# Kernel tuning notes

Hardware: AMD Instinct MI355X
Metric: run time of the kernel (lower is better)

## Reference

```python
import jax, jax.numpy as jnp
import numpy as np

HEADS, LEVELS, POINTS, DIMS = 8, 4, 4, 256
CH = DIMS // HEADS
SHAPES = np.array([[96, 96], [48, 48], [24, 24], [12, 12]], dtype=np.int64)
LEVEL_START = np.concatenate([[0], np.cumsum(SHAPES[:, 0] * SHAPES[:, 1])[:-1]]).astype(np.int64)
HW = int((SHAPES[:, 0] * SHAPES[:, 1]).sum())
N, Q = 2, HW


def setup_inputs() -> dict:
    key = jax.random.key(0)
    ks = jax.random.split(key, 8)
    return {
        "q": jax.random.normal(ks[0], (N, Q, DIMS), jnp.float32),
        "p": jax.random.uniform(ks[1], (N, Q, LEVELS, 2), jnp.float32),
        "v": jax.random.normal(ks[2], (N, HW, DIMS), jnp.float32),
        "W_off": jax.random.normal(ks[3], (DIMS, HEADS * LEVELS * POINTS * 2), jnp.float32) * 0.01,
        "b_off": jax.random.normal(ks[4], (HEADS * LEVELS * POINTS * 2,), jnp.float32) * 0.5,
        "W_attn": jax.random.normal(ks[5], (DIMS, HEADS * LEVELS * POINTS), jnp.float32) * 0.02,
        "b_attn": jnp.zeros((HEADS * LEVELS * POINTS,), jnp.float32),
        "W_in": jax.random.normal(ks[6], (DIMS, DIMS), jnp.float32) / np.float32(np.sqrt(DIMS)),
        "b_in": jnp.zeros((DIMS,), jnp.float32),
        "W_out": jax.random.normal(ks[7], (DIMS, DIMS), jnp.float32) / np.float32(np.sqrt(DIMS)),
        "b_out": jnp.zeros((DIMS,), jnp.float32),
        "shapes": jnp.asarray(SHAPES),
        "level_index": jnp.asarray(LEVEL_START),
    }


def _sample_level(vl, loc_l, Hl, Wl):
    """Bilinear sample with zero padding outside the feature map.
    vl: [N, Hl*Wl, heads, C]; loc_l: [N, Q, heads, P, 2] normalized (x, y) in [0,1].
    Returns [N, Q, P, heads, C]."""
    Nb, Qn, Hd, P, _ = loc_l.shape
    x = loc_l[..., 0] * Wl - 0.5  # pixel coords, align_corners=False convention
    y = loc_l[..., 1] * Hl - 0.5
    x0 = jnp.floor(x)
    y0 = jnp.floor(y)
    dx = x - x0
    dy = y - y0
    x0i = x0.astype(jnp.int32)
    y0i = y0.astype(jnp.int32)
    out = jnp.zeros((Nb, Qn, P, Hd, vl.shape[-1]), vl.dtype)
    corners = ((x0i, y0i, (1 - dx) * (1 - dy)), (x0i + 1, y0i, dx * (1 - dy)),
               (x0i, y0i + 1, (1 - dx) * dy), (x0i + 1, y0i + 1, dx * dy))
    for cx, cy, w in corners:
        valid = (cx >= 0) & (cx < Wl) & (cy >= 0) & (cy < Hl)
        idx = jnp.clip(cy, 0, Hl - 1) * Wl + jnp.clip(cx, 0, Wl - 1)  # [N,Q,Hd,P]
        idx_t = idx.transpose(0, 1, 3, 2).reshape(Nb, Qn * P, Hd, 1)
        g = jnp.take_along_axis(vl, idx_t, axis=1).reshape(Nb, Qn, P, Hd, -1)
        wv = jnp.where(valid, w, 0.0).transpose(0, 1, 3, 2)  # [N,Q,P,Hd]
        out = out + g * wv[..., None].astype(vl.dtype)
    return out


def _forward(q, p, v, W_off, b_off, W_attn, b_attn, W_in, b_in, W_out, b_out, shp, lsi):
    Nb, Qn, _ = q.shape
    v = (v @ W_in + b_in).reshape(Nb, -1, HEADS, CH)
    off = (q @ W_off + b_off).reshape(Nb, Qn, HEADS, LEVELS, POINTS, 2)
    attn = jax.nn.softmax((q @ W_attn + b_attn).reshape(Nb, Qn, HEADS, LEVELS * POINTS), axis=-1)
    attn = attn.reshape(Nb, Qn, HEADS, LEVELS, POINTS)
    # offsets normalized by (W, H) of each level, added to reference points (2-coord branch)
    off_norm = jnp.asarray(np.stack([shp[:, 1], shp[:, 0]], -1), q.dtype)  # [L, 2]
    loc = p[:, :, None, :, None, :] + off / off_norm[None, None, None, :, None, :]  # [N,Q,Hd,L,P,2]
    out = jnp.zeros((Nb, Qn, HEADS, CH), q.dtype)
    for l in range(LEVELS):
        Hl, Wl = int(shp[l, 0]), int(shp[l, 1])
        s = int(lsi[l])
        vl = jax.lax.slice_in_dim(v, s, s + Hl * Wl, axis=1)
        samp = _sample_level(vl, loc[:, :, :, l], Hl, Wl)  # [N,Q,P,Hd,C]
        out = out + jnp.einsum('nqphc,nqhp->nqhc', samp, attn[:, :, :, l])
    return out.reshape(Nb, Qn, DIMS) @ W_out + b_out


def reference(q, p, v, W_off, b_off, W_attn, b_attn, W_in, b_in, W_out, b_out, shapes, level_index):
    shp = np.asarray(shapes)  # spatial shapes are structural constants
    lsi = np.asarray(level_index)
    return _forward(q, p, v, W_off, b_off, W_attn, b_attn, W_in, b_in, W_out, b_out, shp, lsi)
```

## Files before the change

### kernel.cpp

```cpp
#include <hip/hip_runtime.h>
#include <hip/hip_bf16.h>
#include <math.h>

#define NB      2
#define QN      12240
#define HW_TOT  12240
#define DIMS    256
#define HEADS   8
#define CH      32
#define LEVELS  4
#define POINTS  4
#define M_TOT   (NB * QN)

typedef unsigned short ushort_t;
typedef __attribute__((ext_vector_type(8))) short short8;
typedef __attribute__((ext_vector_type(4))) float floatx4;

__device__ __constant__ int c_Hl[4]    = {96, 48, 24, 12};
__device__ __constant__ int c_Wl[4]    = {96, 48, 24, 12};
__device__ __constant__ int c_start[4] = {0, 9216, 11520, 12096};

__device__ __forceinline__ ushort_t f2bf(float f) {
    __hip_bfloat16 h = __float2bfloat16(f);
    return *reinterpret_cast<ushort_t*>(&h);
}

__global__ __launch_bounds__(256) void convert_qv_kernel(
    const float* __restrict__ v, const float* __restrict__ q,
    ushort_t* __restrict__ vbf, ushort_t* __restrict__ qbf)
{
    const size_t i = ((size_t)blockIdx.x * 256 + threadIdx.x) * 8;
    const size_t half = (size_t)M_TOT * DIMS;
    const float* src; ushort_t* dst; size_t off;
    if (i < half) { src = v; dst = vbf; off = i; }
    else          { src = q; dst = qbf; off = i - half; }
    const float4 a = *(const float4*)&src[off];
    const float4 b = *(const float4*)&src[off + 4];
    ushort_t t[8] = {f2bf(a.x), f2bf(a.y), f2bf(a.z), f2bf(a.w),
                     f2bf(b.x), f2bf(b.y), f2bf(b.z), f2bf(b.w)};
    *(int4*)&dst[off] = *(int4*)t;
}

__global__ __launch_bounds__(256) void prep_weights_kernel(
    const float* __restrict__ W_in, const float* __restrict__ W_off,
    const float* __restrict__ W_attn, const float* __restrict__ W_out,
    const float* __restrict__ b_off, const float* __restrict__ b_attn,
    ushort_t* __restrict__ Tin, ushort_t* __restrict__ Tcomb,
    ushort_t* __restrict__ Tout, float* __restrict__ bcomb)
{
    const int z  = blockIdx.z;
    const int gi = blockIdx.x * 256 + threadIdx.x;
    if (z == 1 && gi < 384)
        bcomb[gi] = (gi < 256) ? b_off[gi] : b_attn[gi - 256];
    const int Nw = (z == 1) ? 384 : 256;
    if (gi >= Nw * 256) return;
    const int k = gi & 255;
    const int n = gi >> 8;
    float val; ushort_t* T;
    if (z == 0)      { val = W_in[k * 256 + n];  T = Tin;  }
    else if (z == 1) { val = (n < 256) ? W_off[k * 256 + n]
                                       : W_attn[k * 128 + (n - 256)]; T = Tcomb; }
    else             { val = W_out[k * 256 + n]; T = Tout; }
    T[n * 256 + k] = f2bf(val);
}

__device__ __forceinline__ void gemm_tile_core(
    const ushort_t* __restrict__ A, const ushort_t* __restrict__ BT,
    const float* __restrict__ bias, void* __restrict__ C, bool c_bf16,
    int M, int Nc, int bm0, int bn0, int K,
    ushort_t* As, ushort_t* Bs)
{
    const int tid  = threadIdx.x;
    const int wave = tid >> 6;
    const int lane = tid & 63;
    const int quad = lane >> 4;
    const int l16  = lane & 15;
    const int wm   = (wave >> 1) * 64;
    const int wn   = (wave & 1) * 64;

    const int off0 = tid * 16;
    const int row0 = off0 >> 6;
    const int kc0  = (off0 & 63) >> 1;

    int ar0 = bm0 + row0;      if (ar0 > M - 1) ar0 = M - 1;
    int ar1 = bm0 + row0 + 64; if (ar1 > M - 1) ar1 = M - 1;

    const ushort_t* ga0 = A  + (size_t)ar0 * K + kc0;
    const ushort_t* ga1 = A  + (size_t)ar1 * K + kc0;
    const ushort_t* gb0 = BT + (size_t)(bn0 + row0) * K + kc0;
    const ushort_t* gb1 = BT + (size_t)(bn0 + row0 + 64) * K + kc0;

    ushort_t* lA0 = As + wave * 512;
    ushort_t* lA1 = As + wave * 512 + 2048;
    ushort_t* lB0 = Bs + wave * 512;
    ushort_t* lB1 = Bs + wave * 512 + 2048;

    floatx4 acc[4][4];
    #pragma unroll
    for (int i = 0; i < 4; ++i)
        #pragma unroll
        for (int j = 0; j < 4; ++j)
            acc[i][j] = (floatx4){0.f, 0.f, 0.f, 0.f};

    for (int kk = 0; kk < K; kk += 32) {
        __builtin_amdgcn_global_load_lds(
            (const __attribute__((address_space(1))) void*)(ga0 + kk),
            (__attribute__((address_space(3))) void*)lA0, 16, 0, 0);
        __builtin_amdgcn_global_load_lds(
            (const __attribute__((address_space(1))) void*)(ga1 + kk),
            (__attribute__((address_space(3))) void*)lA1, 16, 0, 0);
        __builtin_amdgcn_global_load_lds(
            (const __attribute__((address_space(1))) void*)(gb0 + kk),
            (__attribute__((address_space(3))) void*)lB0, 16, 0, 0);
        __builtin_amdgcn_global_load_lds(
            (const __attribute__((address_space(1))) void*)(gb1 + kk),
            (__attribute__((address_space(3))) void*)lB1, 16, 0, 0);
        __syncthreads();

        short8 af[4], bfr[4];
        #pragma unroll
        for (int mt = 0; mt < 4; ++mt)
            af[mt] = *(const short8*)&As[(wm + mt * 16 + l16) * 32 + quad * 8];
        #pragma unroll
        for (int nt = 0; nt < 4; ++nt)
            bfr[nt] = *(const short8*)&Bs[(wn + nt * 16 + l16) * 32 + quad * 8];
        #pragma unroll
        for (int mt = 0; mt < 4; ++mt)
            #pragma unroll
            for (int nt = 0; nt < 4; ++nt)
                acc[mt][nt] = __builtin_amdgcn_mfma_f32_16x16x32_bf16(
                    af[mt], bfr[nt], acc[mt][nt], 0, 0, 0);
        __syncthreads();
    }

    #pragma unroll
    for (int mt = 0; mt < 4; ++mt) {
        #pragma unroll
        for (int j = 0; j < 4; ++j) {
            const int row = bm0 + wm + mt * 16 + quad * 4 + j;
            if (row >= M) continue;
            #pragma unroll
            for (int nt = 0; nt < 4; ++nt) {
                const int col = bn0 + wn + nt * 16 + l16;
                const float val = acc[mt][nt][j] + bias[col];
                if (c_bf16) ((ushort_t*)C)[(size_t)row * Nc + col] = f2bf(val);
                else        ((float*)C)[(size_t)row * Nc + col]    = val;
            }
        }
    }
}

__global__ __launch_bounds__(256) void gemm_proj_kernel(
    const ushort_t* __restrict__ vbf, const ushort_t* __restrict__ qbf,
    const ushort_t* __restrict__ Tin, const ushort_t* __restrict__ Tcomb,
    const float* __restrict__ b_in, const float* __restrict__ bcomb,
    ushort_t* __restrict__ vproj, float* __restrict__ offlog)
{
    __shared__ ushort_t As[128 * 32];
    __shared__ ushort_t Bs[128 * 32];
    const int bm0 = blockIdx.x * 128;
    const int y = blockIdx.y;
    if (y < 2)
        gemm_tile_core(vbf, Tin, b_in, vproj, true, M_TOT, 256, bm0, y * 128, 256, As, Bs);
    else
        gemm_tile_core(qbf, Tcomb, bcomb, offlog, false, M_TOT, 384, bm0, (y - 2) * 128, 256, As, Bs);
}

__global__ __launch_bounds__(256) void gemm_out_kernel(
    const ushort_t* __restrict__ mid, const ushort_t* __restrict__ Tout,
    const float* __restrict__ b_out, float* __restrict__ out)
{
    __shared__ ushort_t As[128 * 32];
    __shared__ ushort_t Bs[128 * 32];
    gemm_tile_core(mid, Tout, b_out, out, false, M_TOT, 256,
                   blockIdx.x * 128, blockIdx.y * 128, 256, As, Bs);
}

#define QB 2
#define SLOTS 576

__global__ __launch_bounds__(128) void msda_sample_kernel(
    const ushort_t* __restrict__ vproj, const float* __restrict__ offlog,
    const float* __restrict__ p, ushort_t* __restrict__ mid)
{
    __shared__ float s_logit[QB][128];
    __shared__ float s_off[QB][256];
    __shared__ float s_p[QB][8];
    __shared__ float s_mx[QB][HEADS];
    __shared__ float s_inv[QB][HEADS];
    __shared__ float s_w[QB][SLOTS];
    __shared__ int   s_idx[QB][SLOTS];

    const int tid = threadIdx.x;
    const int bq0 = blockIdx.x * QB;

    #pragma unroll
    for (int i = tid; i < QB * 256; i += 128) {
        int sub = i >> 8, j = i & 255;
        s_off[sub][j] = offlog[(size_t)(bq0 + sub) * 384 + j];
    }
    #pragma unroll
    for (int i = tid; i < QB * 128; i += 128) {
        int sub = i >> 7, j = i & 127;
        s_logit[sub][j] = offlog[(size_t)(bq0 + sub) * 384 + 256 + j];
    }
    if (tid < QB * 8) {
        int sub = tid >> 3, j = tid & 7;
        s_p[sub][j] = p[(size_t)(bq0 + sub) * 8 + j];
    }
    __syncthreads();

    if (tid < QB * HEADS) {
        int sub = tid >> 3, h = tid & 7;
        float mx = -1e30f;
        #pragma unroll
        for (int i = 0; i < 16; ++i) mx = fmaxf(mx, s_logit[sub][h * 16 + i]);
        float ssum = 0.0f;
        #pragma unroll
        for (int i = 0; i < 16; ++i) ssum += __expf(s_logit[sub][h * 16 + i] - mx);
        s_mx[sub][h] = mx;
        s_inv[sub][h] = 1.0f / ssum;
    }
    __syncthreads();

    #pragma unroll
    for (int tt = tid; tt < QB * 128; tt += 128) {
        const int sub = tt >> 7;
        const int j   = tt & 127;
        const int h   = j >> 4;
        const int l   = (j >> 2) & 3;
        const int nq  = bq0 + sub;
        const int nb  = (nq >= QN) ? 1 : 0;

        const int Hl = c_Hl[l], Wl = c_Wl[l], st = c_start[l];
        const float fW = (float)Wl, fH = (float)Hl;

        const float w = __expf(s_logit[sub][j] - s_mx[sub][h]) * s_inv[sub][h];

        const int oi = j * 2;
        const float ox = s_off[sub][oi];
        const float oy = s_off[sub][oi + 1];
        const float px = s_p[sub][l * 2 + 0];
        const float py = s_p[sub][l * 2 + 1];

        const float lx = px + ox / fW;
        const float ly = py + oy / fH;
        const float x = lx * fW - 0.5f;
        const float y = ly * fH - 0.5f;

        const float x0f = floorf(x), y0f = floorf(y);
        const int x0 = (int)x0f, y0 = (int)y0f;
        const float dx = x - x0f, dy = y - y0f;

        const int base = nb * (HW_TOT * DIMS) + h * CH;
        const int slot = (j & 15) * 36 + h * 4;

        const bool vx0 = (x0 >= 0) & (x0 < Wl);
        const bool vx1 = (x0 + 1 >= 0) & (x0 + 1 < Wl);
        const bool vy0 = (y0 >= 0) & (y0 < Hl);
        const bool vy1 = (y0 + 1 >= 0) & (y0 + 1 < Hl);

        s_w[sub][slot + 0] = (vx0 & vy0) ? w * (1.0f - dx) * (1.0f - dy) : 0.0f;
        s_w[sub][slot + 1] = (vx1 & vy0) ? w * dx * (1.0f - dy) : 0.0f;
        s_w[sub][slot + 2] = (vx0 & vy1) ? w * (1.0f - dx) * dy : 0.0f;
        s_w[sub][slot + 3] = (vx1 & vy1) ? w * dx * dy : 0.0f;
        s_idx[sub][slot + 0] = (vx0 & vy0) ? base + (st + y0 * Wl + x0) * DIMS : 0;
        s_idx[sub][slot + 1] = (vx1 & vy0) ? base + (st + y0 * Wl + x0 + 1) * DIMS : 0;
        s_idx[sub][slot + 2] = (vx0 & vy1) ? base + (st + (y0 + 1) * Wl + x0) * DIMS : 0;
        s_idx[sub][slot + 3] = (vx1 & vy1) ? base + (st + (y0 + 1) * Wl + x0 + 1) * DIMS : 0;
    }
    __syncthreads();

    const int sub  = tid >> 6;
    const int lane = tid & 63;
    const int h    = lane >> 3;
    const int c4   = lane & 7;
    const int nq   = bq0 + sub;

    float ax = 0.0f, ay = 0.0f, az = 0.0f, aw = 0.0f;
    const ushort_t* __restrict__ vb = vproj + c4 * 4;

    #pragma unroll
    for (int t = 0; t < 16; ++t) {
        const int slot = t * 36 + h * 4;
        const int4   I = *(const int4*)&s_idx[sub][slot];
        const float4 W = *(const float4*)&s_w[sub][slot];

        const uint2 g0 = *(const uint2*)(vb + I.x);
        const uint2 g1 = *(const uint2*)(vb + I.y);
        const uint2 g2 = *(const uint2*)(vb + I.z);
        const uint2 g3 = *(const uint2*)(vb + I.w);

        ax = fmaf(W.x, __uint_as_float(g0.x << 16), ax);
        ay = fmaf(W.x, __uint_as_float(g0.x & 0xffff0000u), ay);
        az = fmaf(W.x, __uint_as_float(g0.y << 16), az);
        aw = fmaf(W.x, __uint_as_float(g0.y & 0xffff0000u), aw);

        ax = fmaf(W.y, __uint_as_float(g1.x << 16), ax);
        ay = fmaf(W.y, __uint_as_float(g1.x & 0xffff0000u), ay);
        az = fmaf(W.y, __uint_as_float(g1.y << 16), az);
        aw = fmaf(W.y, __uint_as_float(g1.y & 0xffff0000u), aw);

        ax = fmaf(W.z, __uint_as_float(g2.x << 16), ax);
        ay = fmaf(W.z, __uint_as_float(g2.x & 0xffff0000u), ay);
        az = fmaf(W.z, __uint_as_float(g2.y << 16), az);
        aw = fmaf(W.z, __uint_as_float(g2.y & 0xffff0000u), aw);

        ax = fmaf(W.w, __uint_as_float(g3.x << 16), ax);
        ay = fmaf(W.w, __uint_as_float(g3.x & 0xffff0000u), ay);
        az = fmaf(W.w, __uint_as_float(g3.y << 16), az);
        aw = fmaf(W.w, __uint_as_float(g3.y & 0xffff0000u), aw);
    }

    ushort_t mv[4] = {f2bf(ax), f2bf(ay), f2bf(az), f2bf(aw)};
    *(uint2*)&mid[(size_t)nq * DIMS + lane * 4] = *(uint2*)mv;
}

extern "C" void kernel_launch(void* const* d_in, const int* in_sizes, int n_in,
                              void* d_out, int out_size, void* d_ws, size_t ws_size,
                              hipStream_t stream)
{
    const float* q      = (const float*)d_in[0];
    const float* p      = (const float*)d_in[1];
    const float* v      = (const float*)d_in[2];
    const float* W_off  = (const float*)d_in[3];
    const float* b_off  = (const float*)d_in[4];
    const float* W_attn = (const float*)d_in[5];
    const float* b_attn = (const float*)d_in[6];
    const float* W_in   = (const float*)d_in[7];
    const float* b_in   = (const float*)d_in[8];
    const float* W_out  = (const float*)d_in[9];
    const float* b_out  = (const float*)d_in[10];
    float* out = (float*)d_out;

    const int M = M_TOT;

    ushort_t* vproj  = (ushort_t*)d_ws;
    float*    offlog = (float*)(vproj + (size_t)M * 256);
    ushort_t* vbf    = (ushort_t*)(offlog + (size_t)M * 384);
    ushort_t* mid    = vbf;
    ushort_t* qbf    = vbf + (size_t)M * 256;
    ushort_t* Tin    = qbf + (size_t)M * 256;
    ushort_t* Tcomb  = Tin + 256 * 256;
    ushort_t* Tout   = Tcomb + 384 * 256;
    float*    bcomb  = (float*)(Tout + 256 * 256);

    convert_qv_kernel<<<dim3(6120), 256, 0, stream>>>(v, q, vbf, qbf);
    prep_weights_kernel<<<dim3(384, 1, 3), 256, 0, stream>>>(
        W_in, W_off, W_attn, W_out, b_off, b_attn, Tin, Tcomb, Tout, bcomb);

    gemm_proj_kernel<<<dim3(192, 5), 256, 0, stream>>>(
        vbf, qbf, Tin, Tcomb, b_in, bcomb, vproj, offlog);
    msda_sample_kernel<<<dim3(M / QB), 128, 0, stream>>>(vproj, offlog, p, mid);
    gemm_out_kernel<<<dim3(192, 2), 256, 0, stream>>>(mid, Tout, b_out, out);
}
```

Measured before the change: 207.8 us.

## Restructure sampling kernel to one wave per query with shuffle softmax

The sampling kernel now gives each 64-lane wave one query, with four queries per 256-thread block. The softmax max and sum are computed with xor shuffles in registers instead of shared-memory passes. Weights and indices are packed together into a swizzled shared buffer, and block-wide __syncthreads is replaced by a wave barrier plus an LDS waitcnt. Level sizes and start offsets are computed arithmetically instead of read from constant memory. This is meant to cut barrier, shared-memory and per-query setup overhead in exchange for a wave-local synchronization assumption and more complex index arithmetic.

```diff
diff --git a/kernel.cpp b/kernel.cpp
--- a/kernel.cpp
+++ b/kernel.cpp
@@ -15,10 +15,6 @@
 typedef unsigned short ushort_t;
 typedef __attribute__((ext_vector_type(8))) short short8;
 typedef __attribute__((ext_vector_type(4))) float floatx4;
-
-__device__ __constant__ int c_Hl[4]    = {96, 48, 24, 12};
-__device__ __constant__ int c_Wl[4]    = {96, 48, 24, 12};
-__device__ __constant__ int c_start[4] = {0, 9216, 11520, 12096};
 
 __device__ __forceinline__ ushort_t f2bf(float f) {
     __hip_bfloat16 h = __float2bfloat16(f);
@@ -176,144 +172,124 @@
                    blockIdx.x * 128, blockIdx.y * 128, 256, As, Bs);
 }
 
-#define QB 2
-#define SLOTS 576
-
-__global__ __launch_bounds__(128) void msda_sample_kernel(
+#define ACC4(W, g) \
+    ax = fmaf(W, __uint_as_float(g.x << 16), ax);          \
+    ay = fmaf(W, __uint_as_float(g.x & 0xffff0000u), ay);  \
+    az = fmaf(W, __uint_as_float(g.y << 16), az);          \
+    aw = fmaf(W, __uint_as_float(g.y & 0xffff0000u), aw);
+
+__global__ __launch_bounds__(256, 8) void msda_sample_kernel(
     const ushort_t* __restrict__ vproj, const float* __restrict__ offlog,
     const float* __restrict__ p, ushort_t* __restrict__ mid)
 {
-    __shared__ float s_logit[QB][128];
-    __shared__ float s_off[QB][256];
-    __shared__ float s_p[QB][8];
-    __shared__ float s_mx[QB][HEADS];
-    __shared__ float s_inv[QB][HEADS];
-    __shared__ float s_w[QB][SLOTS];
-    __shared__ int   s_idx[QB][SLOTS];
+    __shared__ int s_buf[4096];
 
     const int tid = threadIdx.x;
-    const int bq0 = blockIdx.x * QB;
-
-    #pragma unroll
-    for (int i = tid; i < QB * 256; i += 128) {
-        int sub = i >> 8, j = i & 255;
-        s_off[sub][j] = offlog[(size_t)(bq0 + sub) * 384 + j];
-    }
-    #pragma unroll
-    for (int i = tid; i < QB * 128; i += 128) {
-        int sub = i >> 7, j = i & 127;
-        s_logit[sub][j] = offlog[(size_t)(bq0 + sub) * 384 + 256 + j];
-    }
-    if (tid < QB * 8) {
-        int sub = tid >> 3, j = tid & 7;
-        s_p[sub][j] = p[(size_t)(bq0 + sub) * 8 + j];
-    }
-    __syncthreads();
-
-    if (tid < QB * HEADS) {
-        int sub = tid >> 3, h = tid & 7;
-        float mx = -1e30f;
-        #pragma unroll
-        for (int i = 0; i < 16; ++i) mx = fmaxf(mx, s_logit[sub][h * 16 + i]);
-        float ssum = 0.0f;
-        #pragma unroll
-        for (int i = 0; i < 16; ++i) ssum += __expf(s_logit[sub][h * 16 + i] - mx);
-        s_mx[sub][h] = mx;
-        s_inv[sub][h] = 1.0f / ssum;
-    }
-    __syncthreads();
-
-    #pragma unroll
-    for (int tt = tid; tt < QB * 128; tt += 128) {
-        const int sub = tt >> 7;
-        const int j   = tt & 127;
-        const int h   = j >> 4;
-        const int l   = (j >> 2) & 3;
-        const int nq  = bq0 + sub;
-        const int nb  = (nq >= QN) ? 1 : 0;
-
-        const int Hl = c_Hl[l], Wl = c_Wl[l], st = c_start[l];
-        const float fW = (float)Wl, fH = (float)Hl;
-
-        const float w = __expf(s_logit[sub][j] - s_mx[sub][h]) * s_inv[sub][h];
-
-        const int oi = j * 2;
-        const float ox = s_off[sub][oi];
-        const float oy = s_off[sub][oi + 1];
-        const float px = s_p[sub][l * 2 + 0];
-        const float py = s_p[sub][l * 2 + 1];
-
-        const float lx = px + ox / fW;
-        const float ly = py + oy / fH;
-        const float x = lx * fW - 0.5f;
-        const float y = ly * fH - 0.5f;
-
-        const float x0f = floorf(x), y0f = floorf(y);
-        const int x0 = (int)x0f, y0 = (int)y0f;
-        const float dx = x - x0f, dy = y - y0f;
-
-        const int base = nb * (HW_TOT * DIMS) + h * CH;
-        const int slot = (j & 15) * 36 + h * 4;
-
-        const bool vx0 = (x0 >= 0) & (x0 < Wl);
-        const bool vx1 = (x0 + 1 >= 0) & (x0 + 1 < Wl);
-        const bool vy0 = (y0 >= 0) & (y0 < Hl);
-        const bool vy1 = (y0 + 1 >= 0) & (y0 + 1 < Hl);
-
-        s_w[sub][slot + 0] = (vx0 & vy0) ? w * (1.0f - dx) * (1.0f - dy) : 0.0f;
-        s_w[sub][slot + 1] = (vx1 & vy0) ? w * dx * (1.0f - dy) : 0.0f;
-        s_w[sub][slot + 2] = (vx0 & vy1) ? w * (1.0f - dx) * dy : 0.0f;
-        s_w[sub][slot + 3] = (vx1 & vy1) ? w * dx * dy : 0.0f;
-        s_idx[sub][slot + 0] = (vx0 & vy0) ? base + (st + y0 * Wl + x0) * DIMS : 0;
-        s_idx[sub][slot + 1] = (vx1 & vy0) ? base + (st + y0 * Wl + x0 + 1) * DIMS : 0;
-        s_idx[sub][slot + 2] = (vx0 & vy1) ? base + (st + (y0 + 1) * Wl + x0) * DIMS : 0;
-        s_idx[sub][slot + 3] = (vx1 & vy1) ? base + (st + (y0 + 1) * Wl + x0 + 1) * DIMS : 0;
-    }
-    __syncthreads();
-
-    const int sub  = tid >> 6;
-    const int lane = tid & 63;
-    const int h    = lane >> 3;
-    const int c4   = lane & 7;
-    const int nq   = bq0 + sub;
-
-    float ax = 0.0f, ay = 0.0f, az = 0.0f, aw = 0.0f;
-    const ushort_t* __restrict__ vb = vproj + c4 * 4;
-
-    #pragma unroll
+    const int wv  = tid >> 6;
+    const int l   = tid & 63;
+    const int nq  = blockIdx.x * 4 + wv;
+    const int nb  = (nq >= QN) ? 1 : 0;
+
+    const size_t orow = (size_t)nq * 384;
+    const float2 off0 = *(const float2*)&offlog[orow + 2 * l];
+    const float2 off1 = *(const float2*)&offlog[orow + 128 + 2 * l];
+    const float  lg0  = offlog[orow + 256 + l];
+    const float  lg1  = offlog[orow + 320 + l];
+    const int    lvl  = (l >> 2) & 3;
+    const float2 pl   = *(const float2*)&p[(size_t)nq * 8 + lvl * 2];
+
+    float m0 = lg0, m1 = lg1;
+    #pragma unroll
+    for (int m = 8; m; m >>= 1) {
+        m0 = fmaxf(m0, __shfl_xor(m0, m));
+        m1 = fmaxf(m1, __shfl_xor(m1, m));
+    }
+    const float e0 = __expf(lg0 - m0);
+    const float e1 = __expf(lg1 - m1);
+    float s0 = e0, s1 = e1;
+    #pragma unroll
+    for (int m = 8; m; m >>= 1) {
+        s0 += __shfl_xor(s0, m);
+        s1 += __shfl_xor(s1, m);
+    }
+    const float wt0 = e0 * __builtin_amdgcn_rcpf(s0);
+    const float wt1 = e1 * __builtin_amdgcn_rcpf(s1);
+
+    const int   Wl    = 96 >> lvl;
+    const float fW    = (float)Wl;
+    const int   st    = 12288 - (12288 >> (2 * lvl));
+    const int   h4    = l >> 4;
+    const int   baseb = nb * (HW_TOT * 512) + st * 512;
+    const int   sw    = h4 << 3;
+    const int   wbase = wv * 1024 + l * 8;
+
+    #pragma unroll
+    for (int set = 0; set < 2; ++set) {
+        const float ox = set ? off1.x : off0.x;
+        const float oy = set ? off1.y : off0.y;
+        const float wt = set ? wt1 : wt0;
+        const int   h  = set ? (h4 + 4) : h4;
+
+        const float x  = fmaf(pl.x, fW, ox) - 0.5f;
+        const float y  = fmaf(pl.y, fW, oy) - 0.5f;
+        const float xf = floorf(x), yf = floorf(y);
+        const float dx = x - xf,    dy = y - yf;
+        const int   x0 = (int)xf,   y0 = (int)yf;
+        const bool vx0 = (unsigned)x0       < (unsigned)Wl;
+        const bool vx1 = (unsigned)(x0 + 1) < (unsigned)Wl;
+        const bool vy0 = (unsigned)y0       < (unsigned)Wl;
+        const bool vy1 = (unsigned)(y0 + 1) < (unsigned)Wl;
+
+        const int b00 = baseb + (y0 * Wl + x0) * 512 + h * 64;
+        const int b01 = b00 + 512;
+        const int b10 = b00 + (Wl << 9);
+        const int b11 = b10 + 512;
+
+        const float wy0f = wt * (1.0f - dy), wy1f = wt * dy;
+        const float w00 = (vx0 && vy0) ? (1.0f - dx) * wy0f : 0.0f;
+        const float w01 = (vx1 && vy0) ? dx * wy0f          : 0.0f;
+        const float w10 = (vx0 && vy1) ? (1.0f - dx) * wy1f : 0.0f;
+        const float w11 = (vx1 && vy1) ? dx * wy1f          : 0.0f;
+        const int   i00 = (vx0 && vy0) ? b00 : 0;
+        const int   i01 = (vx1 && vy0) ? b01 : 0;
+        const int   i10 = (vx0 && vy1) ? b10 : 0;
+        const int   i11 = (vx1 && vy1) ? b11 : 0;
+
+        const int o = (wbase + set * 512) ^ sw;
+        *(int4*)&s_buf[o]     = (int4){__float_as_int(w00), i00, __float_as_int(w01), i01};
+        *(int4*)&s_buf[o + 4] = (int4){__float_as_int(w10), i10, __float_as_int(w11), i11};
+    }
+
+    __builtin_amdgcn_wave_barrier();
+    asm volatile("s_waitcnt lgkmcnt(0)" ::: "memory");
+    __builtin_amdgcn_wave_barrier();
+
+    const int h   = l >> 3;
+    const int c4  = l & 7;
+    const int rb  = wv * 1024 + (h >> 2) * 512 + (h & 3) * 128;
+    const int sw2 = (h & 3) << 3;
+    const char* __restrict__ vb = (const char*)vproj;
+
+    float ax = 0.f, ay = 0.f, az = 0.f, aw = 0.f;
+    #pragma unroll 2
     for (int t = 0; t < 16; ++t) {
-        const int slot = t * 36 + h * 4;
-        const int4   I = *(const int4*)&s_idx[sub][slot];
-        const float4 W = *(const float4*)&s_w[sub][slot];
-
-        const uint2 g0 = *(const uint2*)(vb + I.x);
-        const uint2 g1 = *(const uint2*)(vb + I.y);
-        const uint2 g2 = *(const uint2*)(vb + I.z);
-        const uint2 g3 = *(const uint2*)(vb + I.w);
-
-        ax = fmaf(W.x, __uint_as_float(g0.x << 16), ax);
-        ay = fmaf(W.x, __uint_as_float(g0.x & 0xffff0000u), ay);
-        az = fmaf(W.x, __uint_as_float(g0.y << 16), az);
-        aw = fmaf(W.x, __uint_as_float(g0.y & 0xffff0000u), aw);
-
-        ax = fmaf(W.y, __uint_as_float(g1.x << 16), ax);
-        ay = fmaf(W.y, __uint_as_float(g1.x & 0xffff0000u), ay);
-        az = fmaf(W.y, __uint_as_float(g1.y << 16), az);
-        aw = fmaf(W.y, __uint_as_float(g1.y & 0xffff0000u), aw);
-
-        ax = fmaf(W.z, __uint_as_float(g2.x << 16), ax);
-        ay = fmaf(W.z, __uint_as_float(g2.x & 0xffff0000u), ay);
-        az = fmaf(W.z, __uint_as_float(g2.y << 16), az);
-        aw = fmaf(W.z, __uint_as_float(g2.y & 0xffff0000u), aw);
-
-        ax = fmaf(W.w, __uint_as_float(g3.x << 16), ax);
-        ay = fmaf(W.w, __uint_as_float(g3.x & 0xffff0000u), ay);
-        az = fmaf(W.w, __uint_as_float(g3.y << 16), az);
-        aw = fmaf(W.w, __uint_as_float(g3.y & 0xffff0000u), aw);
+        const int o = rb + ((t * 8) ^ sw2);
+        const int4 cA = *(const int4*)&s_buf[o];
+        const int4 cB = *(const int4*)&s_buf[o + 4];
+        const uint2 g0 = *(const uint2*)(vb + (unsigned)(cA.y + c4 * 8));
+        const uint2 g1 = *(const uint2*)(vb + (unsigned)(cA.w + c4 * 8));
+        const uint2 g2 = *(const uint2*)(vb + (unsigned)(cB.y + c4 * 8));
+        const uint2 g3 = *(const uint2*)(vb + (unsigned)(cB.w + c4 * 8));
+        const float W0 = __int_as_float(cA.x), W1 = __int_as_float(cA.z);
+        const float W2 = __int_as_float(cB.x), W3 = __int_as_float(cB.z);
+        ACC4(W0, g0);
+        ACC4(W1, g1);
+        ACC4(W2, g2);
+        ACC4(W3, g3);
     }
 
     ushort_t mv[4] = {f2bf(ax), f2bf(ay), f2bf(az), f2bf(aw)};
-    *(uint2*)&mid[(size_t)nq * DIMS + lane * 4] = *(uint2*)mv;
+    *(uint2*)&mid[(size_t)nq * 256 + l * 4] = *(uint2*)mv;
 }
 
 extern "C" void kernel_launch(void* const* d_in, const int* in_sizes, int n_in,
@@ -351,6 +327,6 @@
 
     gemm_proj_kernel<<<dim3(192, 5), 256, 0, stream>>>(
         vbf, qbf, Tin, Tcomb, b_in, bcomb, vproj, offlog);
-    msda_sample_kernel<<<dim3(M / QB), 128, 0, stream>>>(vproj, offlog, p, mid);
+    msda_sample_kernel<<<dim3(M / 4), 256, 0, stream>>>(vproj, offlog, p, mid);
     gemm_out_kernel<<<dim3(192, 2), 256, 0, stream>>>(mid, Tout, b_out, out);
 }
```

Result: faster. 197.3 us (-5.1%).
